# Kernel tuning notes

Hardware: AMD Instinct MI355X
Metric: run time of the kernel (lower is better)

## Reference

```python
import jax, jax.numpy as jnp
import numpy as np

B, C, H, W = 2, 4, 32, 256   # batch, num_classes (class 0 = background), range-image H x W
N = H * W                    # candidate points per (batch, class)
RADIUS = 3.0
KM_ITERS = 1
COORD_SCALE = 60.0           # spread lidar x/y so radius-3 NMS is non-trivial


def setup_inputs() -> dict:
    key = jax.random.key(0)
    k1, k2 = jax.random.split(key)
    segmented_channels = jax.random.normal(k1, (B, C, H, W), dtype=jnp.float32)
    lidar = jax.random.normal(k2, (B, 2, H, W), dtype=jnp.float32) * COORD_SCALE
    return {"segmented_channels": segmented_channels, "lidar": lidar}


def _radius_nms(points, mask, radius):
    # Greedy radius NMS in index order: keep point i iff no earlier kept point
    # lies within `radius`. Masked-out points are never kept (keep init = mask).
    n = points.shape[0]
    idx = jnp.arange(n)
    r2 = radius * radius

    def step(keep, i):
        d2 = jnp.sum((points - points[i]) ** 2, axis=-1)       # [N]
        suppress = keep & (d2 < r2) & (idx > i) & keep[i]
        return keep & ~suppress, None

    keep, _ = jax.lax.scan(step, mask, idx)
    return keep


def _kmeans(points, mask, keep, iters):
    # Centers initialized at the NMS-kept points (same index space as points).
    # Each valid class point is assigned to nearest valid center; centers move
    # to the mean of their assigned points.
    n = points.shape[0]
    centers = points
    w = mask.astype(points.dtype)
    BIG = jnp.asarray(1e30, points.dtype)
    for _ in range(iters):
        d2 = jnp.sum((points[:, None, :] - centers[None, :, :]) ** 2, axis=-1)  # [N,N]
        d2 = jnp.where(keep[None, :], d2, BIG)
        assign = jnp.argmin(d2, axis=1)                         # [N]
        sums = jax.ops.segment_sum(points * w[:, None], assign, num_segments=n)
        cnt = jax.ops.segment_sum(w, assign, num_segments=n)
        upd = sums / jnp.maximum(cnt, 1.0)[:, None]
        centers = jnp.where((keep & (cnt > 0))[:, None], upd, centers)
    return centers * keep[:, None].astype(points.dtype)


def reference(segmented_channels, lidar):
    ind = jnp.argmax(segmented_channels, axis=1)                # [B,H,W] class id per cell
    pts = jnp.stack([lidar[:, 0], lidar[:, 1]], axis=-1).reshape(B, N, 2)
    # boolean class masks for foreground classes 1..C-1
    cls_mask = jnp.stack([ind == c for c in range(1, C)], axis=1).reshape(B, C - 1, N)
    pts_all = jnp.broadcast_to(pts[:, None], (B, C - 1, N, 2)).reshape(B * (C - 1), N, 2)
    mask_all = cls_mask.reshape(B * (C - 1), N)

    def per_bc(args):
        p, m = args
        keep = _radius_nms(p, m, RADIUS)
        centers = _kmeans(p, m, keep, KM_ITERS)
        return centers, keep

    centers, keep = jax.lax.map(per_bc, (pts_all, mask_all))
    # centers: padded [B, C-1, N, 2]; keep marks which rows are real detections
    return centers.reshape(B, C - 1, N, 2), keep.reshape(B, C - 1, N)
```

## Files before the change

### kernel.cpp

```cpp
#include <hip/hip_runtime.h>

#define NPTS 8192
#define BCLS 4
#define NP   6
#define R2   9.0f
#define RAD  3.0f
#define GRD  64
#define NCELL (GRD*GRD)
#define PCAP 2048
#define LDSK 2048

#define ST_U 0
#define ST_A 1
#define ST_D 2

__global__ __launch_bounds__(1024) void k_fused(
    const float* __restrict__ seg, const float* __restrict__ lidar,
    float* __restrict__ sumx, float* __restrict__ sumy, float* __restrict__ cntw,
    float* __restrict__ out)
{
    const int p = blockIdx.x;
    const int b = p / 3, cls = p % 3 + 1;
    const int tid = threadIdx.x, lane = tid & 63, wv = tid >> 6;
    const int base = p * NPTS;

    __shared__ float2 sp[NPTS];
    __shared__ unsigned short cidx[NPTS];
    __shared__ unsigned short sortid[NPTS];
    __shared__ unsigned int cellpack[NCELL];
    __shared__ unsigned char st[NPTS];
    __shared__ unsigned short plist[2][PCAP];
    __shared__ float ksx[LDSK], ksy[LDSK], kcn[LDSK];
    __shared__ int pcnt[2];
    __shared__ unsigned long long ballots[128];
    __shared__ unsigned int base128[128];
    __shared__ unsigned int wtot[16];
    __shared__ float redbuf[4][16];
    __shared__ float sbminx, sbminy, scell;
    __shared__ int sM, sK;

    float* ok = out + (size_t)2 * NP * NPTS + base;

    for (int k = tid; k < NPTS; k += 1024) { st[k] = ST_U; ok[k] = 0.f; }
    {
        float2* oc = (float2*)(out + (size_t)2 * base);
        for (int k = tid; k < NPTS; k += 1024) oc[k] = make_float2(0.f, 0.f);
    }
    for (int k = tid; k < NCELL; k += 1024) cellpack[k] = 0u;
    for (int k = tid; k < LDSK; k += 1024) { ksx[k] = 0.f; ksy[k] = 0.f; kcn[k] = 0.f; }
    if (tid == 0) { pcnt[0] = 0; pcnt[1] = 0; }

    const float* segb = seg + (size_t)b * BCLS * NPTS;
    const float* lx = lidar + (size_t)b * 2 * NPTS;
    const float* ly = lx + NPTS;
    for (int c0 = 0; c0 < 8; ++c0) {
        int n = c0 * 1024 + tid;
        float bv = segb[n];
        int bc = 0;
        #pragma unroll
        for (int c2 = 1; c2 < BCLS; ++c2) {
            float v = segb[c2 * NPTS + n];
            if (v > bv) { bv = v; bc = c2; }
        }
        unsigned long long bal = __ballot(bc == cls);
        if (lane == 0) ballots[c0 * 16 + wv] = bal;
    }
    __syncthreads();
    if (wv == 0) {
        unsigned int p0 = (unsigned int)__popcll(ballots[2 * lane]);
        unsigned int p1 = (unsigned int)__popcll(ballots[2 * lane + 1]);
        unsigned int s = p0 + p1, v = s;
        for (int d = 1; d < 64; d <<= 1) {
            unsigned int u = __shfl_up(v, d, 64);
            if (lane >= d) v += u;
        }
        base128[2 * lane] = v - s;
        base128[2 * lane + 1] = v - p1;
        if (lane == 63) sM = (int)v;
    }
    __syncthreads();
    const int M = sM;
    for (int c0 = 0; c0 < 8; ++c0) {
        unsigned long long bal = ballots[c0 * 16 + wv];
        if ((bal >> lane) & 1ull) {
            int n = c0 * 1024 + tid;
            int pos = (int)base128[c0 * 16 + wv] + __popcll(bal & ((1ull << lane) - 1ull));
            sp[pos] = make_float2(lx[n], ly[n]);
            cidx[pos] = (unsigned short)n;
        }
    }
    __syncthreads();

    {
        float mnx = 3e38f, mxx = -3e38f, mny = 3e38f, mxy = -3e38f;
        for (int i = tid; i < M; i += 1024) {
            float2 q = sp[i];
            mnx = fminf(mnx, q.x); mxx = fmaxf(mxx, q.x);
            mny = fminf(mny, q.y); mxy = fmaxf(mxy, q.y);
        }
        for (int d = 32; d; d >>= 1) {
            mnx = fminf(mnx, __shfl_xor(mnx, d, 64));
            mxx = fmaxf(mxx, __shfl_xor(mxx, d, 64));
            mny = fminf(mny, __shfl_xor(mny, d, 64));
            mxy = fmaxf(mxy, __shfl_xor(mxy, d, 64));
        }
        if (lane == 0) { redbuf[0][wv] = mnx; redbuf[1][wv] = mxx;
                         redbuf[2][wv] = mny; redbuf[3][wv] = mxy; }
    }
    __syncthreads();
    if (tid == 0) {
        float a = redbuf[0][0], b2 = redbuf[1][0], c = redbuf[2][0], d = redbuf[3][0];
        for (int q = 1; q < 16; ++q) {
            a = fminf(a, redbuf[0][q]); b2 = fmaxf(b2, redbuf[1][q]);
            c = fminf(c, redbuf[2][q]); d = fmaxf(d, redbuf[3][q]);
        }
        sbminx = a; sbminy = c;
        scell = fmaxf(2.0f * RAD, fmaxf(b2 - a, d - c) / 63.0f);
    }
    __syncthreads();
    const float bminx = sbminx, bminy = sbminy, inv = 1.0f / scell;

    for (int i = tid; i < M; i += 1024) {
        float2 q = sp[i];
        int ix = min(GRD - 1, max(0, (int)((q.x - bminx) * inv)));
        int iy = min(GRD - 1, max(0, (int)((q.y - bminy) * inv)));
        atomicAdd(&cellpack[iy * GRD + ix], 1u);
    }
    __syncthreads();
    {
        unsigned int c4[4], t4 = 0;
        #pragma unroll
        for (int q = 0; q < 4; ++q) { c4[q] = cellpack[tid * 4 + q]; t4 += c4[q]; }
        unsigned int v = t4;
        for (int d = 1; d < 64; d <<= 1) {
            unsigned int u = __shfl_up(v, d, 64);
            if (lane >= d) v += u;
        }
        if (lane == 63) wtot[wv] = v;
        __syncthreads();
        if (tid == 0) {
            unsigned int acc = 0;
            for (int q = 0; q < 16; ++q) { unsigned int t = wtot[q]; wtot[q] = acc; acc += t; }
        }
        __syncthreads();
        unsigned int excl = wtot[wv] + v - t4;
        #pragma unroll
        for (int q = 0; q < 4; ++q) { cellpack[tid * 4 + q] = excl << 16; excl += c4[q]; }
    }
    __syncthreads();
    for (int i = tid; i < M; i += 1024) {
        float2 q = sp[i];
        int ix = min(GRD - 1, max(0, (int)((q.x - bminx) * inv)));
        int iy = min(GRD - 1, max(0, (int)((q.y - bminy) * inv)));
        unsigned int old = atomicAdd(&cellpack[iy * GRD + ix], 1u);
        sortid[(old >> 16) + (old & 0xffffu)] = (unsigned short)i;
    }
    __syncthreads();

    #define ROW_FLAGS(CY, CX0, CX1, I, ME, DEAD, UNDEC)                           \
    {                                                                             \
        unsigned int wa = cellpack[(CY) * GRD + (CX0)];                           \
        unsigned int wb = cellpack[(CY) * GRD + (CX1)];                           \
        unsigned int e0 = wa >> 16, e1 = (wb >> 16) + (wb & 0xffffu);             \
        for (unsigned int e = e0; e < e1; ++e) {                                  \
            int j = sortid[e];                                                    \
            float2 q = sp[j];                                                     \
            unsigned char sv = st[j];                                             \
            float dx = __fsub_rn(ME.x, q.x), dy = __fsub_rn(ME.y, q.y);           \
            float d2 = __fadd_rn(__fmul_rn(dx, dx), __fmul_rn(dy, dy));           \
            bool in = (d2 < R2) & (j < (I));                                      \
            DEAD  |= in & (sv == ST_A);                                           \
            UNDEC |= in & (sv == ST_U);                                           \
        }                                                                         \
    }
    #define SCAN_FLAGS(I, ME, DEAD, UNDEC)                                        \
    {                                                                             \
        int cx0 = max(0, (int)((ME.x - RAD - bminx) * inv));                      \
        int cx1 = min(GRD - 1, (int)((ME.x + RAD - bminx) * inv));                \
        int cy0 = max(0, (int)((ME.y - RAD - bminy) * inv));                      \
        int cy1 = min(GRD - 1, (int)((ME.y + RAD - bminy) * inv));                \
        DEAD = false; UNDEC = false;                                              \
        ROW_FLAGS(cy0, cx0, cx1, I, ME, DEAD, UNDEC);                             \
        if (cy1 > cy0) ROW_FLAGS(cy1, cx0, cx1, I, ME, DEAD, UNDEC);              \
    }

    for (int g = tid; g < M; g += 1024) {
        int i = sortid[g];
        float2 me = sp[i];
        bool dead, undec;
        SCAN_FLAGS(i, me, dead, undec);
        if (dead) st[i] = ST_D;
        else if (!undec) st[i] = ST_A;
        bool pendf = !dead && undec;
        unsigned long long act = __ballot(true);
        unsigned long long bal = __ballot(pendf);
        int leader = __builtin_ctzll(act);
        int cnt = __popcll(bal);
        int wbase = 0;
        if (lane == leader && cnt) wbase = atomicAdd(&pcnt[0], cnt);
        wbase = __shfl(wbase, leader, 64);
        if (pendf) {
            int pos = wbase + __popcll(bal & ((1ull << lane) - 1ull));
            if (pos < PCAP) plist[0][pos] = (unsigned short)i;
        }
    }

    int cur = 0;
    for (int round = 0; round < NPTS; ++round) {
        __syncthreads();
        int pc = pcnt[cur];
        if (pc == 0) break;
        if (pc > PCAP) {
            for (;;) {
                bool any = false;
                __syncthreads();
                for (int i = tid; i < M; i += 1024) {
                    if (st[i] != ST_U) continue;
                    float2 me = sp[i];
                    bool dead, undec;
                    SCAN_FLAGS(i, me, dead, undec);
                    if (dead) st[i] = ST_D;
                    else if (!undec) st[i] = ST_A;
                    else any = true;
                }
                if (__syncthreads_count(any) == 0) break;
            }
            break;
        }
        if (tid == 0) pcnt[cur ^ 1] = 0;
        __syncthreads();
        for (int idx = tid; idx < pc; idx += 1024) {
            int i = plist[cur][idx];
            float2 me = sp[i];
            bool dead, undec;
            SCAN_FLAGS(i, me, dead, undec);
            if (dead) st[i] = ST_D;
            else if (!undec) st[i] = ST_A;
            bool pendf = !dead && undec;
            unsigned long long act = __ballot(true);
            unsigned long long bal = __ballot(pendf);
            int leader = __builtin_ctzll(act);
            int cnt = __popcll(bal);
            int wbase = 0;
            if (lane == leader && cnt) wbase = atomicAdd(&pcnt[cur ^ 1], cnt);
            wbase = __shfl(wbase, leader, 64);
            if (pendf) {
                int pos = wbase + __popcll(bal & ((1ull << lane) - 1ull));
                if (pos < PCAP) plist[cur ^ 1][pos] = (unsigned short)i;
            }
        }
        cur ^= 1;
    }
    __syncthreads();

    for (int k = 0; k < 8; ++k) {
        int i = (k << 10) + tid;
        unsigned long long bal = __ballot(st[i] == ST_A);
        if (lane == 0) ballots[(k << 4) + wv] = bal;
    }
    __syncthreads();
    if (wv == 0) {
        unsigned int p0 = (unsigned int)__popcll(ballots[2 * lane]);
        unsigned int p1 = (unsigned int)__popcll(ballots[2 * lane + 1]);
        unsigned int s = p0 + p1, v = s;
        for (int d = 1; d < 64; d <<= 1) {
            unsigned int u = __shfl_up(v, d, 64);
            if (lane >= d) v += u;
        }
        base128[2 * lane] = v - s;
        base128[2 * lane + 1] = v - p1;
        if (lane == 63) sK = (int)v;
    }
    __syncthreads();
    #define KRANK(J) ((int)base128[(J) >> 6] +                                    \
                      __popcll(ballots[(J) >> 6] & ((1ull << ((J) & 63)) - 1ull)))
    if (sK > LDSK) {
        for (int k = tid; k < NPTS; k += 1024) {
            sumx[base + k] = 0.f; sumy[base + k] = 0.f; cntw[base + k] = 0.f;
        }
        __syncthreads();
    }

    #define ROW_ARGMIN(CY, CX0, CX1, ME, BD, BJ)                                  \
    {                                                                             \
        unsigned int wa = cellpack[(CY) * GRD + (CX0)];                           \
        unsigned int wb = cellpack[(CY) * GRD + (CX1)];                           \
        unsigned int e0 = wa >> 16, e1 = (wb >> 16) + (wb & 0xffffu);             \
        for (unsigned int e = e0; e < e1; ++e) {                                  \
            int j = sortid[e];                                                    \
            float2 q = sp[j];                                                     \
            unsigned char sv = st[j];                                             \
            float dx = __fsub_rn(ME.x, q.x), dy = __fsub_rn(ME.y, q.y);           \
            float d2 = __fadd_rn(__fmul_rn(dx, dx), __fmul_rn(dy, dy));           \
            bool better = (sv == ST_A) & ((d2 < BD) | ((d2 == BD) & (j < BJ)));   \
            BD = better ? d2 : BD;                                                \
            BJ = better ? j : BJ;                                                 \
        }                                                                         \
    }
    for (int g = tid; g < M; g += 1024) {
        int i = sortid[g];
        float2 me = sp[i];
        int bj;
        if (st[i] == ST_A) {
            bj = i;
        } else {
            int cx0 = max(0, (int)((me.x - RAD - bminx) * inv));
            int cx1 = min(GRD - 1, (int)((me.x + RAD - bminx) * inv));
            int cy0 = max(0, (int)((me.y - RAD - bminy) * inv));
            int cy1 = min(GRD - 1, (int)((me.y + RAD - bminy) * inv));
            float bd = 3e38f;
            bj = -1;
            ROW_ARGMIN(cy0, cx0, cx1, me, bd, bj);
            if (cy1 > cy0) ROW_ARGMIN(cy1, cx0, cx1, me, bd, bj);
            if (bj < 0) continue;
        }
        int r = KRANK(bj);
        if (r < LDSK) {
            atomicAdd(&ksx[r], me.x);
            atomicAdd(&ksy[r], me.y);
            atomicAdd(&kcn[r], 1.0f);
        } else {
            atomicAdd(&sumx[base + bj], me.x);
            atomicAdd(&sumy[base + bj], me.y);
            atomicAdd(&cntw[base + bj], 1.0f);
        }
    }
    __syncthreads();

    for (int i = tid; i < M; i += 1024) {
        if (st[i] != ST_A) continue;
        int n = cidx[i];
        int r = KRANK(i);
        float sx, sy, c;
        if (r < LDSK) { sx = ksx[r]; sy = ksy[r]; c = kcn[r]; }
        else { sx = sumx[base + i]; sy = sumy[base + i]; c = cntw[base + i]; }
        out[2 * (base + n)]     = sx / c;
        out[2 * (base + n) + 1] = sy / c;
        ok[n] = 1.0f;
    }
}

extern "C" void kernel_launch(void* const* d_in, const int* in_sizes, int n_in,
                              void* d_out, int out_size, void* d_ws, size_t ws_size,
                              hipStream_t stream) {
    const float* seg   = (const float*)d_in[0];
    const float* lidar = (const float*)d_in[1];
    float* out = (float*)d_out;

    const size_t A = (size_t)NP * NPTS;
    float* sumx = (float*)d_ws;
    float* sumy = sumx + A;
    float* cntw = sumy + A;

    k_fused<<<NP, 1024, 0, stream>>>(seg, lidar, sumx, sumy, cntw, out);
}
```

Measured before the change: 109.5 us.

## Replace barrier-synchronized NMS rounds with asynchronous per-thread spin resolution

Replaces the round-based pending-list NMS, which used block barriers and atomics to compact undecided points each round, with a barrier-free scheme. Each thread owns up to eight points and repeatedly rescans them, reading neighbour states through volatile LDS loads until every owned point is decided. A barrier-synchronized fallback sweep guarantees completion. This removes per-round __syncthreads and list compaction, but relies on cross-wave LDS visibility without fences and can spin wastefully when dependency chains are long.

New measurement: 123.1 us. +12.4%, slower.

```diff
diff --git a/kernel.cpp b/kernel.cpp
--- a/kernel.cpp
+++ b/kernel.cpp
@@ -7,8 +7,8 @@
 #define RAD  3.0f
 #define GRD  64
 #define NCELL (GRD*GRD)
-#define PCAP 2048
 #define LDSK 2048
+#define OWNMAX 8
 
 #define ST_U 0
 #define ST_A 1
@@ -29,9 +29,7 @@
     __shared__ unsigned short sortid[NPTS];
     __shared__ unsigned int cellpack[NCELL];
     __shared__ unsigned char st[NPTS];
-    __shared__ unsigned short plist[2][PCAP];
     __shared__ float ksx[LDSK], ksy[LDSK], kcn[LDSK];
-    __shared__ int pcnt[2];
     __shared__ unsigned long long ballots[128];
     __shared__ unsigned int base128[128];
     __shared__ unsigned int wtot[16];
@@ -39,6 +37,7 @@
     __shared__ float sbminx, sbminy, scell;
     __shared__ int sM, sK;
 
+    volatile unsigned char* vst = (volatile unsigned char*)st;
     float* ok = out + (size_t)2 * NP * NPTS + base;
 
     for (int k = tid; k < NPTS; k += 1024) { st[k] = ST_U; ok[k] = 0.f; }
@@ -48,7 +47,6 @@
     }
     for (int k = tid; k < NCELL; k += 1024) cellpack[k] = 0u;
     for (int k = tid; k < LDSK; k += 1024) { ksx[k] = 0.f; ksy[k] = 0.f; kcn[k] = 0.f; }
-    if (tid == 0) { pcnt[0] = 0; pcnt[1] = 0; }
 
     const float* segb = seg + (size_t)b * BCLS * NPTS;
     const float* lx = lidar + (size_t)b * 2 * NPTS;
@@ -165,7 +163,7 @@
         for (unsigned int e = e0; e < e1; ++e) {                                  \
             int j = sortid[e];                                                    \
             float2 q = sp[j];                                                     \
-            unsigned char sv = st[j];                                             \
+            unsigned char sv = vst[j];                                            \
             float dx = __fsub_rn(ME.x, q.x), dy = __fsub_rn(ME.y, q.y);           \
             float d2 = __fadd_rn(__fmul_rn(dx, dx), __fmul_rn(dy, dy));           \
             bool in = (d2 < R2) & (j < (I));                                      \
@@ -184,74 +182,42 @@
         if (cy1 > cy0) ROW_FLAGS(cy1, cx0, cx1, I, ME, DEAD, UNDEC);              \
     }
 
-    for (int g = tid; g < M; g += 1024) {
-        int i = sortid[g];
-        float2 me = sp[i];
-        bool dead, undec;
-        SCAN_FLAGS(i, me, dead, undec);
-        if (dead) st[i] = ST_D;
-        else if (!undec) st[i] = ST_A;
-        bool pendf = !dead && undec;
-        unsigned long long act = __ballot(true);
-        unsigned long long bal = __ballot(pendf);
-        int leader = __builtin_ctzll(act);
-        int cnt = __popcll(bal);
-        int wbase = 0;
-        if (lane == leader && cnt) wbase = atomicAdd(&pcnt[0], cnt);
-        wbase = __shfl(wbase, leader, 64);
-        if (pendf) {
-            int pos = wbase + __popcll(bal & ((1ull << lane) - 1ull));
-            if (pos < PCAP) plist[0][pos] = (unsigned short)i;
-        }
-    }
-
-    int cur = 0;
-    for (int round = 0; round < NPTS; ++round) {
-        __syncthreads();
-        int pc = pcnt[cur];
-        if (pc == 0) break;
-        if (pc > PCAP) {
-            for (;;) {
-                bool any = false;
-                __syncthreads();
-                for (int i = tid; i < M; i += 1024) {
-                    if (st[i] != ST_U) continue;
-                    float2 me = sp[i];
-                    bool dead, undec;
-                    SCAN_FLAGS(i, me, dead, undec);
-                    if (dead) st[i] = ST_D;
-                    else if (!undec) st[i] = ST_A;
-                    else any = true;
-                }
-                if (__syncthreads_count(any) == 0) break;
+    {
+        int own[OWNMAX];
+        float2 ops[OWNMAX];
+        int nown = 0;
+        for (int g = tid; g < M; g += 1024) {
+            int i = sortid[g];
+            own[nown] = i;
+            ops[nown] = sp[i];
+            ++nown;
+        }
+        int nres = 0;
+        for (int spin = 0; nres < nown && spin < (1 << 17); ++spin) {
+            for (int k = 0; k < nown; ++k) {
+                int i = own[k];
+                if (i < 0) continue;
+                float2 me = ops[k];
+                bool dead, undec;
+                SCAN_FLAGS(i, me, dead, undec);
+                if (dead)       { st[i] = ST_D; own[k] = -1; ++nres; }
+                else if (!undec){ st[i] = ST_A; own[k] = -1; ++nres; }
             }
-            break;
-        }
-        if (tid == 0) pcnt[cur ^ 1] = 0;
-        __syncthreads();
-        for (int idx = tid; idx < pc; idx += 1024) {
-            int i = plist[cur][idx];
+        }
+    }
+    for (;;) {
+        bool any = false;
+        for (int i = tid; i < M; i += 1024) {
+            if (st[i] != ST_U) continue;
             float2 me = sp[i];
             bool dead, undec;
             SCAN_FLAGS(i, me, dead, undec);
             if (dead) st[i] = ST_D;
             else if (!undec) st[i] = ST_A;
-            bool pendf = !dead && undec;
-            unsigned long long act = __ballot(true);
-            unsigned long long bal = __ballot(pendf);
-            int leader = __builtin_ctzll(act);
-            int cnt = __popcll(bal);
-            int wbase = 0;
-            if (lane == leader && cnt) wbase = atomicAdd(&pcnt[cur ^ 1], cnt);
-            wbase = __shfl(wbase, leader, 64);
-            if (pendf) {
-                int pos = wbase + __popcll(bal & ((1ull << lane) - 1ull));
-                if (pos < PCAP) plist[cur ^ 1][pos] = (unsigned short)i;
-            }
-        }
-        cur ^= 1;
-    }
-    __syncthreads();
+            else any = true;
+        }
+        if (__syncthreads_count(any) == 0) break;
+    }
 
     for (int k = 0; k < 8; ++k) {
         int i = (k << 10) + tid;
```
